# Kernel tuning notes

Hardware: AMD Instinct MI355X
Metric: run time of the kernel (lower is better)

The kernel has to match this reference:

```python
import jax, jax.numpy as jnp
import numpy as np


def _build_K(seq_length, kernel_size):
    """Replicates MovingAvgTime's banded matrix construction + nearest-exact
    interpolation along the column axis, then transpose.
    Final K[j, a] = 1/k if starts[j] <= a < starts[j] + k else 0, where
    starts[j] = floor((j + 0.5) * (L - k + 1) / L) clamped (nearest-exact)."""
    L, k = seq_length, kernel_size
    n_cols = L - k + 1
    j = jnp.arange(L, dtype=jnp.float32)
    # nearest-exact index map from output size L back to input size n_cols
    starts = jnp.minimum(((j + 0.5) * (n_cols / L)).astype(jnp.int32), n_cols - 1)  # [L]
    a = jnp.arange(L, dtype=jnp.int32)
    band = (a[None, :] >= starts[:, None]) & (a[None, :] < starts[:, None] + k)  # [L, L]
    return band.astype(jnp.float32) / k


def setup_inputs() -> dict:
    key = jax.random.key(0)
    B, L, C = 32, 4096, 64
    x = jax.random.normal(key, (B, L, C), dtype=jnp.float32)
    return {"x": x, "kernel_size": 16}


def reference(x, kernel_size):
    L = x.shape[1]
    K = _build_K(L, kernel_size)           # [L, L] banded moving-average matrix
    # out[b, j, c] = sum_a K[j, a] * x[b, a, c]  (same as torch: self.K @ x)
    return jnp.einsum('ja,bac->bjc', K, x)
```

## Files before the change

### kernel.cpp

```cpp
#include <hip/hip_runtime.h>


#define LL   4096
#define C4   16
#define BJ   64
#define NR   80
#define JPT  4
#define NSTG 5

typedef float v4 __attribute__((ext_vector_type(4)));

__global__ __launch_bounds__(256) void mavg16_kernel(const float* __restrict__ x,
                                                     const int* __restrict__ kptr,
                                                     float* __restrict__ out) {
    __shared__ v4 lds[NR * C4];

    const int k = *kptr;
    const int ncols = LL - k + 1;
    const float cmap = (float)((double)ncols / (double)LL);

    const int nwg = (int)gridDim.x;
    const int cpx = nwg >> 3;
    const int bid = (int)blockIdx.x;
    const int w = (bid & 7) * cpx + (bid >> 3);

    const int b    = w >> 6;
    const int jblk = w & 63;
    const int j0b  = jblk * BJ;

    const int tid = (int)threadIdx.x;
    const int c4  = tid & 15;
    const int jgl = tid >> 4;

    const v4* xb = (const v4*)x + (size_t)b * (LL * C4);
    v4*       ob = (v4*)out     + (size_t)b * (LL * C4);

    if (k == 16) {
        int sbase = (int)(((float)j0b + 0.5f) * cmap);
        sbase = min(sbase, ncols - 1);
        const int base4 = sbase * C4;

        #pragma unroll
        for (int i = 0; i < NSTG; ++i) {
            const int f = i * 256 + tid;
            const int g = min(base4 + f, LL * C4 - 1);
            __builtin_amdgcn_global_load_lds(
                (const __attribute__((address_space(1))) unsigned int*)(xb + g),
                (__attribute__((address_space(3))) unsigned int*)&lds[f],
                16, 0, 0);
        }
        __syncthreads();

        const float inv = 0.0625f;
        const int j0 = j0b + jgl * JPT;
        int s0 = (int)(((float)j0 + 0.5f) * cmap);
        s0 = min(s0, ncols - 1);
        const int r0 = s0 - sbase;

        v4 acc = (v4){0.f, 0.f, 0.f, 0.f};
        #pragma unroll
        for (int t = 0; t < 16; ++t) {
            acc += lds[(r0 + t) * C4 + c4];
        }
        __builtin_nontemporal_store(acc * inv, &ob[(size_t)j0 * C4 + c4]);

        int sp = r0;
        #pragma unroll
        for (int t = 1; t < JPT; ++t) {
            int sn = (int)(((float)(j0 + t) + 0.5f) * cmap);
            sn = min(sn, ncols - 1) - sbase;
            v4 ra = lds[(sn + 15) * C4 + c4];
            v4 rs = lds[sp * C4 + c4];
            if (sn != sp) acc += ra - rs;
            sp = sn;
            __builtin_nontemporal_store(acc * inv, &ob[(size_t)(j0 + t) * C4 + c4]);
        }
    } else {
        const float inv = 1.0f / (float)k;
        for (int t = 0; t < JPT; ++t) {
            const int j = j0b + jgl * JPT + t;
            int s = (int)(((float)j + 0.5f) * cmap);
            s = min(s, ncols - 1);
            v4 acc = (v4){0.f, 0.f, 0.f, 0.f};
            for (int a = 0; a < k; ++a) {
                acc += xb[(size_t)(s + a) * C4 + c4];
            }
            ob[(size_t)j * C4 + c4] = acc * inv;
        }
    }
}

extern "C" void kernel_launch(void* const* d_in, const int* in_sizes, int n_in,
                              void* d_out, int out_size, void* d_ws, size_t ws_size,
                              hipStream_t stream) {
    const float* x    = (const float*)d_in[0];
    const int*   kptr = (const int*)d_in[1];
    float*       out  = (float*)d_out;
    mavg16_kernel<<<dim3(2048), dim3(256), 0, stream>>>(x, kptr, out);
}
```

Before: 14.36 us.

## Process two row tiles per block with double-buffered async LDS loads

Each workgroup now handles two consecutive 64-row tiles. It issues both tiles' global-to-LDS loads up front into separate buffers, then waits on partial vmcnt so the first tile's compute and stores overlap the second tile's loads. The grid is halved to 1024 blocks. In exchange, LDS per block doubles and fewer blocks are available to hide latency, and the hand-written vmcnt counts assume a specific ordering of memory operations.

After: 13.81 us (median of 2 runs). 3.9% less time.

```diff
diff --git a/kernel.cpp b/kernel.cpp
--- a/kernel.cpp
+++ b/kernel.cpp
@@ -13,7 +13,7 @@
 __global__ __launch_bounds__(256) void mavg16_kernel(const float* __restrict__ x,
                                                      const int* __restrict__ kptr,
                                                      float* __restrict__ out) {
-    __shared__ v4 lds[NR * C4];
+    __shared__ v4 lds[2 * NR * C4];
 
     const int k = *kptr;
     const int ncols = LL - k + 1;
@@ -24,9 +24,10 @@
     const int bid = (int)blockIdx.x;
     const int w = (bid & 7) * cpx + (bid >> 3);
 
-    const int b    = w >> 6;
-    const int jblk = w & 63;
-    const int j0b  = jblk * BJ;
+    const int b  = w >> 5;
+    const int pr = w & 31;
+    const int j0_T0 = pr * 128;
+    const int j0_T1 = pr * 128 + 64;
 
     const int tid = (int)threadIdx.x;
     const int c4  = tid & 15;
@@ -36,56 +37,88 @@
     v4*       ob = (v4*)out     + (size_t)b * (LL * C4);
 
     if (k == 16) {
-        int sbase = (int)(((float)j0b + 0.5f) * cmap);
-        sbase = min(sbase, ncols - 1);
-        const int base4 = sbase * C4;
+        int sb0 = min((int)(((float)j0_T0 + 0.5f) * cmap), ncols - 1);
+        int sb1 = min((int)(((float)j0_T1 + 0.5f) * cmap), ncols - 1);
 
         #pragma unroll
         for (int i = 0; i < NSTG; ++i) {
             const int f = i * 256 + tid;
-            const int g = min(base4 + f, LL * C4 - 1);
+            const int g = min(sb0 * C4 + f, LL * C4 - 1);
             __builtin_amdgcn_global_load_lds(
                 (const __attribute__((address_space(1))) unsigned int*)(xb + g),
                 (__attribute__((address_space(3))) unsigned int*)&lds[f],
                 16, 0, 0);
         }
-        __syncthreads();
+        #pragma unroll
+        for (int i = 0; i < NSTG; ++i) {
+            const int f = i * 256 + tid;
+            const int g = min(sb1 * C4 + f, LL * C4 - 1);
+            __builtin_amdgcn_global_load_lds(
+                (const __attribute__((address_space(1))) unsigned int*)(xb + g),
+                (__attribute__((address_space(3))) unsigned int*)&lds[NR * C4 + f],
+                16, 0, 0);
+        }
+
+        asm volatile("s_waitcnt vmcnt(5)" ::: "memory");
+        __builtin_amdgcn_s_barrier();
 
         const float inv = 0.0625f;
-        const int j0 = j0b + jgl * JPT;
-        int s0 = (int)(((float)j0 + 0.5f) * cmap);
-        s0 = min(s0, ncols - 1);
-        const int r0 = s0 - sbase;
 
-        v4 acc = (v4){0.f, 0.f, 0.f, 0.f};
-        #pragma unroll
-        for (int t = 0; t < 16; ++t) {
-            acc += lds[(r0 + t) * C4 + c4];
+        {
+            const v4* buf = lds;
+            const int j0 = j0_T0 + jgl * JPT;
+            int s0 = min((int)(((float)j0 + 0.5f) * cmap), ncols - 1);
+            const int r0 = s0 - sb0;
+            v4 acc = (v4){0.f, 0.f, 0.f, 0.f};
+            #pragma unroll
+            for (int t = 0; t < 16; ++t) acc += buf[(r0 + t) * C4 + c4];
+            __builtin_nontemporal_store(acc * inv, &ob[(size_t)j0 * C4 + c4]);
+            int sp = r0;
+            #pragma unroll
+            for (int t = 1; t < JPT; ++t) {
+                int sn = min((int)(((float)(j0 + t) + 0.5f) * cmap), ncols - 1) - sb0;
+                v4 ra = buf[(sn + 15) * C4 + c4];
+                v4 rs = buf[sp * C4 + c4];
+                if (sn != sp) acc += ra - rs;
+                sp = sn;
+                __builtin_nontemporal_store(acc * inv, &ob[(size_t)(j0 + t) * C4 + c4]);
+            }
         }
-        __builtin_nontemporal_store(acc * inv, &ob[(size_t)j0 * C4 + c4]);
 
-        int sp = r0;
-        #pragma unroll
-        for (int t = 1; t < JPT; ++t) {
-            int sn = (int)(((float)(j0 + t) + 0.5f) * cmap);
-            sn = min(sn, ncols - 1) - sbase;
-            v4 ra = lds[(sn + 15) * C4 + c4];
-            v4 rs = lds[sp * C4 + c4];
-            if (sn != sp) acc += ra - rs;
-            sp = sn;
-            __builtin_nontemporal_store(acc * inv, &ob[(size_t)(j0 + t) * C4 + c4]);
+        asm volatile("s_waitcnt vmcnt(4)" ::: "memory");
+        __builtin_amdgcn_s_barrier();
+
+        {
+            const v4* buf = lds + NR * C4;
+            const int j0 = j0_T1 + jgl * JPT;
+            int s0 = min((int)(((float)j0 + 0.5f) * cmap), ncols - 1);
+            const int r0 = s0 - sb1;
+            v4 acc = (v4){0.f, 0.f, 0.f, 0.f};
+            #pragma unroll
+            for (int t = 0; t < 16; ++t) acc += buf[(r0 + t) * C4 + c4];
+            __builtin_nontemporal_store(acc * inv, &ob[(size_t)j0 * C4 + c4]);
+            int sp = r0;
+            #pragma unroll
+            for (int t = 1; t < JPT; ++t) {
+                int sn = min((int)(((float)(j0 + t) + 0.5f) * cmap), ncols - 1) - sb1;
+                v4 ra = buf[(sn + 15) * C4 + c4];
+                v4 rs = buf[sp * C4 + c4];
+                if (sn != sp) acc += ra - rs;
+                sp = sn;
+                __builtin_nontemporal_store(acc * inv, &ob[(size_t)(j0 + t) * C4 + c4]);
+            }
         }
     } else {
         const float inv = 1.0f / (float)k;
-        for (int t = 0; t < JPT; ++t) {
-            const int j = j0b + jgl * JPT + t;
-            int s = (int)(((float)j + 0.5f) * cmap);
-            s = min(s, ncols - 1);
-            v4 acc = (v4){0.f, 0.f, 0.f, 0.f};
-            for (int a = 0; a < k; ++a) {
-                acc += xb[(size_t)(s + a) * C4 + c4];
+        for (int tile = 0; tile < 2; ++tile) {
+            const int j0b = (tile == 0) ? j0_T0 : j0_T1;
+            for (int t = 0; t < JPT; ++t) {
+                const int j = j0b + jgl * JPT + t;
+                int s = min((int)(((float)j + 0.5f) * cmap), ncols - 1);
+                v4 acc = (v4){0.f, 0.f, 0.f, 0.f};
+                for (int a = 0; a < k; ++a) acc += xb[(size_t)(s + a) * C4 + c4];
+                ob[(size_t)j * C4 + c4] = acc * inv;
             }
-            ob[(size_t)j * C4 + c4] = acc * inv;
         }
     }
 }
@@ -96,5 +129,5 @@
     const float* x    = (const float*)d_in[0];
     const int*   kptr = (const int*)d_in[1];
     float*       out  = (float*)d_out;
-    mavg16_kernel<<<dim3(2048), dim3(256), 0, stream>>>(x, kptr, out);
+    mavg16_kernel<<<dim3(1024), dim3(256), 0, stream>>>(x, kptr, out);
 }
```

## Double-buffer LDS staging across four smaller row tiles per workgroup

Applied to the files above, without the earlier changes.

Each workgroup now processes four 32-row tiles instead of one 64-row tile. Global-to-LDS async loads for the next tile are issued into a second LDS buffer while the current tile is computed, using explicit vmcnt waits and barriers. The grid is halved to 1024 workgroups. The intent is to overlap load latency with compute, at the cost of extra halo reloading (48 rows per 32 outputs instead of 80 per 64), more barriers, and fewer workgroups in flight.

New measurement: 17.03 us. +18.6%, slower.

```diff
diff --git a/kernel.cpp b/kernel.cpp
--- a/kernel.cpp
+++ b/kernel.cpp
@@ -3,17 +3,18 @@
 
 #define LL   4096
 #define C4   16
-#define BJ   64
-#define NR   80
-#define JPT  4
-#define NSTG 5
+#define BJ   32
+#define NR   48
+#define JPT  2
+#define NSTG 3
+#define NT   4
 
 typedef float v4 __attribute__((ext_vector_type(4)));
 
 __global__ __launch_bounds__(256) void mavg16_kernel(const float* __restrict__ x,
                                                      const int* __restrict__ kptr,
                                                      float* __restrict__ out) {
-    __shared__ v4 lds[NR * C4];
+    __shared__ v4 lds[2 * NR * C4];
 
     const int k = *kptr;
     const int ncols = LL - k + 1;
@@ -24,9 +25,9 @@
     const int bid = (int)blockIdx.x;
     const int w = (bid & 7) * cpx + (bid >> 3);
 
-    const int b    = w >> 6;
-    const int jblk = w & 63;
-    const int j0b  = jblk * BJ;
+    const int b     = w >> 5;
+    const int pr    = w & 31;
+    const int jbase = pr * (NT * BJ);
 
     const int tid = (int)threadIdx.x;
     const int c4  = tid & 15;
@@ -36,56 +37,74 @@
     v4*       ob = (v4*)out     + (size_t)b * (LL * C4);
 
     if (k == 16) {
-        int sbase = (int)(((float)j0b + 0.5f) * cmap);
-        sbase = min(sbase, ncols - 1);
-        const int base4 = sbase * C4;
+        int sb[NT];
+        #pragma unroll
+        for (int t = 0; t < NT; ++t)
+            sb[t] = min((int)(((float)(jbase + t * BJ) + 0.5f) * cmap), ncols - 1);
 
-        #pragma unroll
-        for (int i = 0; i < NSTG; ++i) {
-            const int f = i * 256 + tid;
-            const int g = min(base4 + f, LL * C4 - 1);
-            __builtin_amdgcn_global_load_lds(
-                (const __attribute__((address_space(1))) unsigned int*)(xb + g),
-                (__attribute__((address_space(3))) unsigned int*)&lds[f],
-                16, 0, 0);
-        }
-        __syncthreads();
+        auto stage = [&](int sbase, int bufi) {
+            const int base4 = sbase * C4;
+            #pragma unroll
+            for (int i = 0; i < NSTG; ++i) {
+                const int f = i * 256 + tid;
+                const int g = min(base4 + f, LL * C4 - 1);
+                __builtin_amdgcn_global_load_lds(
+                    (const __attribute__((address_space(1))) unsigned int*)(xb + g),
+                    (__attribute__((address_space(3))) unsigned int*)&lds[bufi * (NR * C4) + f],
+                    16, 0, 0);
+            }
+        };
 
-        const float inv = 0.0625f;
-        const int j0 = j0b + jgl * JPT;
-        int s0 = (int)(((float)j0 + 0.5f) * cmap);
-        s0 = min(s0, ncols - 1);
-        const int r0 = s0 - sbase;
+        auto compute = [&](int tilej0, int bufi, int sbase) {
+            const v4* buf = lds + bufi * (NR * C4);
+            const int j0 = tilej0 + jgl * JPT;
+            int s0 = min((int)(((float)j0 + 0.5f) * cmap), ncols - 1);
+            const int r0 = s0 - sbase;
+            v4 acc = (v4){0.f, 0.f, 0.f, 0.f};
+            #pragma unroll
+            for (int t = 0; t < 16; ++t) acc += buf[(r0 + t) * C4 + c4];
+            __builtin_nontemporal_store(acc * 0.0625f, &ob[(size_t)j0 * C4 + c4]);
+            int sn = min((int)(((float)(j0 + 1) + 0.5f) * cmap), ncols - 1) - sbase;
+            v4 ra = buf[(sn + 15) * C4 + c4];
+            v4 rs = buf[r0 * C4 + c4];
+            if (sn != r0) acc += ra - rs;
+            __builtin_nontemporal_store(acc * 0.0625f, &ob[(size_t)(j0 + 1) * C4 + c4]);
+        };
 
-        v4 acc = (v4){0.f, 0.f, 0.f, 0.f};
-        #pragma unroll
-        for (int t = 0; t < 16; ++t) {
-            acc += lds[(r0 + t) * C4 + c4];
-        }
-        __builtin_nontemporal_store(acc * inv, &ob[(size_t)j0 * C4 + c4]);
+        stage(sb[0], 0);
+        stage(sb[1], 1);
 
-        int sp = r0;
-        #pragma unroll
-        for (int t = 1; t < JPT; ++t) {
-            int sn = (int)(((float)(j0 + t) + 0.5f) * cmap);
-            sn = min(sn, ncols - 1) - sbase;
-            v4 ra = lds[(sn + 15) * C4 + c4];
-            v4 rs = lds[sp * C4 + c4];
-            if (sn != sp) acc += ra - rs;
-            sp = sn;
-            __builtin_nontemporal_store(acc * inv, &ob[(size_t)(j0 + t) * C4 + c4]);
-        }
+        asm volatile("s_waitcnt vmcnt(3)" ::: "memory");
+        __builtin_amdgcn_s_barrier();
+        compute(jbase + 0 * BJ, 0, sb[0]);
+        asm volatile("" ::: "memory");
+        __builtin_amdgcn_s_barrier();
+        stage(sb[2], 0);
+
+        asm volatile("s_waitcnt vmcnt(5)" ::: "memory");
+        __builtin_amdgcn_s_barrier();
+        compute(jbase + 1 * BJ, 1, sb[1]);
+        asm volatile("" ::: "memory");
+        __builtin_amdgcn_s_barrier();
+        stage(sb[3], 1);
+
+        asm volatile("s_waitcnt vmcnt(5)" ::: "memory");
+        __builtin_amdgcn_s_barrier();
+        compute(jbase + 2 * BJ, 0, sb[2]);
+
+        asm volatile("s_waitcnt vmcnt(2)" ::: "memory");
+        __builtin_amdgcn_s_barrier();
+        compute(jbase + 3 * BJ, 1, sb[3]);
     } else {
         const float inv = 1.0f / (float)k;
-        for (int t = 0; t < JPT; ++t) {
-            const int j = j0b + jgl * JPT + t;
-            int s = (int)(((float)j + 0.5f) * cmap);
-            s = min(s, ncols - 1);
-            v4 acc = (v4){0.f, 0.f, 0.f, 0.f};
-            for (int a = 0; a < k; ++a) {
-                acc += xb[(size_t)(s + a) * C4 + c4];
+        for (int t = 0; t < NT; ++t) {
+            for (int u = 0; u < JPT; ++u) {
+                const int j = jbase + t * BJ + jgl * JPT + u;
+                int s = min((int)(((float)j + 0.5f) * cmap), ncols - 1);
+                v4 acc = (v4){0.f, 0.f, 0.f, 0.f};
+                for (int a = 0; a < k; ++a) acc += xb[(size_t)(s + a) * C4 + c4];
+                ob[(size_t)j * C4 + c4] = acc * inv;
             }
-            ob[(size_t)j * C4 + c4] = acc * inv;
         }
     }
 }
@@ -96,5 +115,5 @@
     const float* x    = (const float*)d_in[0];
     const int*   kptr = (const int*)d_in[1];
     float*       out  = (float*)d_out;
-    mavg16_kernel<<<dim3(2048), dim3(256), 0, stream>>>(x, kptr, out);
+    mavg16_kernel<<<dim3(1024), dim3(256), 0, stream>>>(x, kptr, out);
 }
```

## Shrink blocks to one wavefront and replace barrier with vmcnt wait

Applied to the files above, without the earlier changes.

Each block becomes a single 64-thread wavefront. Each thread now produces 16 consecutive outputs through the sliding-window update instead of 4, and issues 20 staged LDS loads instead of 5. Because the block is one wave, the __syncthreads barrier is replaced by an s_waitcnt vmcnt(0). This is meant to remove barrier cost and per-thread setup overhead, in exchange for a longer serial dependency chain per thread and fewer threads in flight to hide memory latency. It relies on the global_load_lds data being visible once vmcnt reaches zero, with no further LDS synchronization.

After: 14.20 us. About the same (-1.1%).

```diff
diff --git a/kernel.cpp b/kernel.cpp
--- a/kernel.cpp
+++ b/kernel.cpp
@@ -5,14 +5,14 @@
 #define C4   16
 #define BJ   64
 #define NR   80
-#define JPT  4
-#define NSTG 5
+#define NSTG 20
+#define JPT  16
 
 typedef float v4 __attribute__((ext_vector_type(4)));
 
-__global__ __launch_bounds__(256) void mavg16_kernel(const float* __restrict__ x,
-                                                     const int* __restrict__ kptr,
-                                                     float* __restrict__ out) {
+__global__ __launch_bounds__(64) void mavg16_kernel(const float* __restrict__ x,
+                                                    const int* __restrict__ kptr,
+                                                    float* __restrict__ out) {
     __shared__ v4 lds[NR * C4];
 
     const int k = *kptr;
@@ -24,51 +24,46 @@
     const int bid = (int)blockIdx.x;
     const int w = (bid & 7) * cpx + (bid >> 3);
 
-    const int b    = w >> 6;
-    const int jblk = w & 63;
-    const int j0b  = jblk * BJ;
+    const int b     = w >> 6;
+    const int tile  = w & 63;
+    const int jbase = tile * BJ;
 
     const int tid = (int)threadIdx.x;
     const int c4  = tid & 15;
     const int jgl = tid >> 4;
+    const int j0  = jbase + jgl * JPT;
 
     const v4* xb = (const v4*)x + (size_t)b * (LL * C4);
     v4*       ob = (v4*)out     + (size_t)b * (LL * C4);
 
     if (k == 16) {
-        int sbase = (int)(((float)j0b + 0.5f) * cmap);
-        sbase = min(sbase, ncols - 1);
+        int sbase = min((int)(((float)jbase + 0.5f) * cmap), ncols - 1);
         const int base4 = sbase * C4;
 
         #pragma unroll
         for (int i = 0; i < NSTG; ++i) {
-            const int f = i * 256 + tid;
+            const int f = i * 64 + tid;
             const int g = min(base4 + f, LL * C4 - 1);
             __builtin_amdgcn_global_load_lds(
                 (const __attribute__((address_space(1))) unsigned int*)(xb + g),
                 (__attribute__((address_space(3))) unsigned int*)&lds[f],
                 16, 0, 0);
         }
-        __syncthreads();
+        asm volatile("s_waitcnt vmcnt(0)" ::: "memory");
 
         const float inv = 0.0625f;
-        const int j0 = j0b + jgl * JPT;
-        int s0 = (int)(((float)j0 + 0.5f) * cmap);
-        s0 = min(s0, ncols - 1);
+        int s0 = min((int)(((float)j0 + 0.5f) * cmap), ncols - 1);
         const int r0 = s0 - sbase;
 
         v4 acc = (v4){0.f, 0.f, 0.f, 0.f};
         #pragma unroll
-        for (int t = 0; t < 16; ++t) {
-            acc += lds[(r0 + t) * C4 + c4];
-        }
+        for (int t = 0; t < 16; ++t) acc += lds[(r0 + t) * C4 + c4];
         __builtin_nontemporal_store(acc * inv, &ob[(size_t)j0 * C4 + c4]);
 
         int sp = r0;
         #pragma unroll
         for (int t = 1; t < JPT; ++t) {
-            int sn = (int)(((float)(j0 + t) + 0.5f) * cmap);
-            sn = min(sn, ncols - 1) - sbase;
+            int sn = min((int)(((float)(j0 + t) + 0.5f) * cmap), ncols - 1) - sbase;
             v4 ra = lds[(sn + 15) * C4 + c4];
             v4 rs = lds[sp * C4 + c4];
             if (sn != sp) acc += ra - rs;
@@ -78,13 +73,10 @@
     } else {
         const float inv = 1.0f / (float)k;
         for (int t = 0; t < JPT; ++t) {
-            const int j = j0b + jgl * JPT + t;
-            int s = (int)(((float)j + 0.5f) * cmap);
-            s = min(s, ncols - 1);
+            const int j = j0 + t;
+            int s = min((int)(((float)j + 0.5f) * cmap), ncols - 1);
             v4 acc = (v4){0.f, 0.f, 0.f, 0.f};
-            for (int a = 0; a < k; ++a) {
-                acc += xb[(size_t)(s + a) * C4 + c4];
-            }
+            for (int a = 0; a < k; ++a) acc += xb[(size_t)(s + a) * C4 + c4];
             ob[(size_t)j * C4 + c4] = acc * inv;
         }
     }
@@ -96,5 +88,5 @@
     const float* x    = (const float*)d_in[0];
     const int*   kptr = (const int*)d_in[1];
     float*       out  = (float*)d_out;
-    mavg16_kernel<<<dim3(2048), dim3(256), 0, stream>>>(x, kptr, out);
+    mavg16_kernel<<<dim3(2048), dim3(64), 0, stream>>>(x, kptr, out);
 }
```
